# Kernel tuning notes

Hardware: AMD Instinct MI355X
Metric: run time of the kernel (lower is better)

The kernel has to match this reference:

```python
import jax, jax.numpy as jnp
import numpy as np

EPS = 1e-5


def setup_inputs() -> dict:
    key = jax.random.key(0)
    ks = jax.random.split(key, 5)
    N, E, D, L = 10000, 160000, 512, 3
    x = jax.random.normal(ks[0], (N, D), dtype=jnp.float32)
    src = jax.random.randint(ks[1], (E,), 0, N, dtype=jnp.int64)
    dst = jax.random.randint(ks[2], (E,), 0, N, dtype=jnp.int64)
    gamma = jnp.ones((L, D), dtype=jnp.float32)
    beta = jnp.zeros((L, D), dtype=jnp.float32)
    # glorot-ish scale so ReLU stack stays well-conditioned
    W = jax.random.normal(ks[3], (L, D, D), dtype=jnp.float32) * (1.0 / np.sqrt(D))
    b = jnp.zeros((L, D), dtype=jnp.float32)
    return {"x": x, "src": src, "dst": dst, "gamma": gamma, "beta": beta, "W": W, "b": b}


def reference(x, src, dst, gamma, beta, W, b):
    N = x.shape[0]
    ones = jnp.ones(src.shape[0], dtype=x.dtype)
    # DGL GraphConv norm='both': src side uses out-degree, dst side uses in-degree
    out_deg = jnp.clip(jax.ops.segment_sum(ones, src, num_segments=N), 1.0)
    in_deg = jnp.clip(jax.ops.segment_sum(ones, dst, num_segments=N), 1.0)
    src_norm = (out_deg ** -0.5)[:, None]  # [N,1]
    dst_norm = (in_deg ** -0.5)[:, None]   # [N,1]
    n_layers = gamma.shape[0]
    for i in range(n_layers):
        # BatchNorm1d (training mode: batch mean, biased variance)
        mu = jnp.mean(x, axis=0)
        var = jnp.var(x, axis=0)
        x = (x - mu) * jax.lax.rsqrt(var + EPS) * gamma[i] + beta[i]
        h = x * src_norm
        agg = jax.ops.segment_sum(h[src], dst, num_segments=N) * dst_norm
        x = jax.nn.relu(agg @ W[i] + b[i])
    return x
```

## Files before the change

### kernel.cpp

```cpp
#include <hip/hip_runtime.h>
#include <hip/hip_bf16.h>

constexpr int N = 10000;
constexpr int D = 512;
constexpr int E = 160000;
constexpr int L = 3;
constexpr float EPS = 1e-5f;

typedef _Float16 half8 __attribute__((ext_vector_type(8)));
typedef _Float16 half2v __attribute__((ext_vector_type(2)));
typedef float floatx4 __attribute__((ext_vector_type(4)));

__device__ __forceinline__ void glds16(const _Float16* g, _Float16* l) {
    __builtin_amdgcn_global_load_lds(
        (const __attribute__((address_space(1))) uint32_t*)(g),
        (__attribute__((address_space(3))) uint32_t*)(l),
        16, 0, 0);
}

constexpr int DEG_BLOCKS  = (E + 255) / 256;
constexpr int CONV_BLOCKS = 1000;
constexpr int TW_BLOCKS   = L * 256;
constexpr int MEGA_BLOCKS = DEG_BLOCKS + CONV_BLOCKS + TW_BLOCKS;

__global__ __launch_bounds__(256) void mega_setup(
    const int* __restrict__ src, const int* __restrict__ dst,
    const float* __restrict__ x, const float* __restrict__ W,
    int* __restrict__ out_deg, int* __restrict__ in_deg,
    _Float16* __restrict__ x16, float* __restrict__ stats0,
    _Float16* __restrict__ Wt) {
    __shared__ float tb[32][33];
    int bid = blockIdx.x;
    int tid = threadIdx.x;
    if (bid < DEG_BLOCKS) {
        int e = bid * 256 + tid;
        if (e < E) {
            atomicAdd(&out_deg[src[e]], 1);
            atomicAdd(&in_deg[dst[e]], 1);
        }
    } else if (bid < DEG_BLOCKS + CONV_BLOCKS) {
        int b = bid - DEG_BLOCKS;
        int r0 = b * 10;
        int r1 = r0 + 10; if (r1 > N) r1 = N;
        int c2 = tid * 2;
        float s0 = 0.f, s1 = 0.f, q0 = 0.f, q1 = 0.f;
        for (int r = r0; r < r1; ++r) {
            float2 v = *(const float2*)(x + (size_t)r * D + c2);
            s0 += v.x; q0 += v.x * v.x;
            s1 += v.y; q1 += v.y * v.y;
            half2v h; h[0] = (_Float16)v.x; h[1] = (_Float16)v.y;
            *(half2v*)(x16 + (size_t)r * D + c2) = h;
        }
        atomicAdd(&stats0[c2], s0);
        atomicAdd(&stats0[c2 + 1], s1);
        atomicAdd(&stats0[D + c2], q0);
        atomicAdd(&stats0[D + c2 + 1], q1);
    } else {
        int b = bid - DEG_BLOCKS - CONV_BLOCKS;
        int l = b >> 8;
        int t = b & 255;
        int k0 = (t >> 4) * 32, n0 = (t & 15) * 32;
        int tx = tid & 31, ty = tid >> 5;
        const float* Wl = W + (size_t)l * D * D;
        _Float16* Wtl = Wt + (size_t)l * D * D;
        for (int i = 0; i < 32; i += 8)
            tb[ty + i][tx] = Wl[(size_t)(k0 + ty + i) * D + n0 + tx];
        __syncthreads();
        for (int i = 0; i < 32; i += 8)
            Wtl[(size_t)(n0 + ty + i) * D + k0 + tx] = (_Float16)tb[tx][ty + i];
    }
}

__global__ void scan_indeg(const int* __restrict__ in_deg,
                           const int* __restrict__ out_deg,
                           int* __restrict__ off, int* __restrict__ cursor,
                           float* __restrict__ src_norm, float* __restrict__ dst_norm) {
    __shared__ int lsum[1024];
    int t = threadIdx.x;
    const int chunk = (N + 1023) / 1024;
    int start = t * chunk;
    int end = start + chunk; if (end > N) end = N;
    int s = 0;
    for (int i = start; i < end; ++i) s += in_deg[i];
    lsum[t] = s;
    __syncthreads();
    for (int d = 1; d < 1024; d <<= 1) {
        int v = (t >= d) ? lsum[t - d] : 0;
        __syncthreads();
        lsum[t] += v;
        __syncthreads();
    }
    int excl = (t == 0) ? 0 : lsum[t - 1];
    for (int i = start; i < end; ++i) {
        off[i] = excl;
        cursor[i] = excl;
        excl += in_deg[i];
        int od = out_deg[i]; if (od < 1) od = 1;
        int id = in_deg[i];  if (id < 1) id = 1;
        src_norm[i] = rsqrtf((float)od);
        dst_norm[i] = rsqrtf((float)id);
    }
    if (t == 1023) off[N] = lsum[1023];
}

__global__ void csr_fill(const int* __restrict__ src, const int* __restrict__ dst,
                         int* __restrict__ cursor, int* __restrict__ csr_src) {
    int e = blockIdx.x * blockDim.x + threadIdx.x;
    if (e >= E) return;
    int d = dst[e];
    int pos = atomicAdd(&cursor[d], 1);
    csr_src[pos] = src[e];
}

__global__ __launch_bounds__(256) void aggregate_bn(
    const _Float16* __restrict__ x, const int* __restrict__ off,
    const int* __restrict__ csr_src, const float* __restrict__ src_norm,
    const float* __restrict__ dst_norm, const float* __restrict__ stats,
    const float* __restrict__ gamma, const float* __restrict__ beta,
    _Float16* __restrict__ agg) {
    int wid = (blockIdx.x * 256 + threadIdx.x) >> 6;
    if (wid >= N) return;
    int lane = threadIdx.x & 63;
    int c0 = lane * 8;

    float scale[8], shift[8];
    const float invN = 1.0f / (float)N;
    for (int i = 0; i < 8; ++i) {
        int c = c0 + i;
        float mu = stats[c] * invN;
        float var = stats[D + c] * invN - mu * mu;
        float sc = gamma[c] * rsqrtf(var + EPS);
        scale[i] = sc;
        shift[i] = beta[c] - mu * sc;
    }

    int e0 = off[wid], e1 = off[wid + 1];
    float a[8] = {}, a2[8] = {};
    float t = 0.f;
    int e = e0;
    for (; e + 4 <= e1; e += 4) {
        int s0 = csr_src[e];
        int s1 = csr_src[e + 1];
        int s2 = csr_src[e + 2];
        int s3 = csr_src[e + 3];
        float n0 = src_norm[s0];
        float n1 = src_norm[s1];
        float n2 = src_norm[s2];
        float n3 = src_norm[s3];
        half8 v0 = *(const half8*)(x + (size_t)s0 * D + c0);
        half8 v1 = *(const half8*)(x + (size_t)s1 * D + c0);
        half8 v2 = *(const half8*)(x + (size_t)s2 * D + c0);
        half8 v3 = *(const half8*)(x + (size_t)s3 * D + c0);
        t += (n0 + n1) + (n2 + n3);
        for (int k = 0; k < 8; ++k) {
            a[k]  += (float)v0[k] * n0;
            a2[k] += (float)v1[k] * n1;
            a[k]  += (float)v2[k] * n2;
            a2[k] += (float)v3[k] * n3;
        }
    }
    for (; e < e1; ++e) {
        int s0 = csr_src[e];
        float n0 = src_norm[s0];
        half8 v0 = *(const half8*)(x + (size_t)s0 * D + c0);
        t += n0;
        for (int k = 0; k < 8; ++k) a[k] += (float)v0[k] * n0;
    }
    float dn = dst_norm[wid];
    half8 o;
    for (int i = 0; i < 8; ++i)
        o[i] = (_Float16)(dn * (scale[i] * (a[i] + a2[i]) + shift[i] * t));
    *(half8*)(agg + (size_t)wid * D + c0) = o;
}

template <typename OutT, bool STATS>
__global__ __launch_bounds__(128) void mm_f16_relu(
    const _Float16* __restrict__ A, const _Float16* __restrict__ Bt,
    const float* __restrict__ bias, OutT* __restrict__ C, int M,
    float* __restrict__ stats) {
    __shared__ __align__(16) _Float16 As[2][64 * 64];
    __shared__ __align__(16) _Float16 Bs[2][128 * 64];
    const int tid  = threadIdx.x;
    const int wave = tid >> 6;
    const int lane = tid & 63;
    const int quad = lane >> 4;
    const int l16  = lane & 15;
    const int row0 = blockIdx.x * 64;
    const int col0 = blockIdx.y * 128;
    const int wn   = wave * 64;

    const int srl = lane >> 3;
    const int sq  = lane & 7;
    const int sqs = (sq ^ srl) * 8;

    const _Float16* gA[4];
    const _Float16* gB[8];
#pragma unroll
    for (int j = 0; j < 4; ++j) {
        int ar = row0 + wave * 32 + j * 8 + srl;
        if (ar >= M) ar = M - 1;
        gA[j] = A + (size_t)ar * D + sqs;
    }
#pragma unroll
    for (int j = 0; j < 8; ++j) {
        int br = col0 + wave * 64 + j * 8 + srl;
        gB[j] = Bt + (size_t)br * D + sqs;
    }

    const int l7 = l16 & 7;
    const int swz0 = (quad ^ l7) * 8;
    const int swz1 = ((4 + quad) ^ l7) * 8;

    floatx4 acc[4][4] = {};

    auto stage = [&](int buf, int k0) {
        _Float16* as = As[buf] + (wave * 32) * 64;
        _Float16* bs = Bs[buf] + (wave * 64) * 64;
#pragma unroll
        for (int j = 0; j < 4; ++j)
            glds16(gA[j] + k0, as + j * 8 * 64);
#pragma unroll
        for (int j = 0; j < 8; ++j)
            glds16(gB[j] + k0, bs + j * 8 * 64);
    };

    stage(0, 0);
    __syncthreads();

    int cur = 0;
    for (int kt = 0; kt < 8; ++kt) {
        if (kt < 7) stage(cur ^ 1, (kt + 1) * 64);
        const _Float16* asb = As[cur];
        const _Float16* bsb = Bs[cur];
        half8 af0[4], af1[4], bf0[4], bf1[4];
#pragma unroll
        for (int i = 0; i < 4; ++i) {
            int r = i * 16 + l16;
            af0[i] = *(const half8*)(asb + r * 64 + swz0);
            af1[i] = *(const half8*)(asb + r * 64 + swz1);
        }
#pragma unroll
        for (int j = 0; j < 4; ++j) {
            int r = wn + j * 16 + l16;
            bf0[j] = *(const half8*)(bsb + r * 64 + swz0);
            bf1[j] = *(const half8*)(bsb + r * 64 + swz1);
        }
#pragma unroll
        for (int i = 0; i < 4; ++i)
#pragma unroll
            for (int j = 0; j < 4; ++j)
                acc[i][j] = __builtin_amdgcn_mfma_f32_16x16x32_f16(
                    af0[i], bf0[j], acc[i][j], 0, 0, 0);
#pragma unroll
        for (int i = 0; i < 4; ++i)
#pragma unroll
            for (int j = 0; j < 4; ++j)
                acc[i][j] = __builtin_amdgcn_mfma_f32_16x16x32_f16(
                    af1[i], bf1[j], acc[i][j], 0, 0, 0);
        __syncthreads();
        cur ^= 1;
    }

    float s[4] = {}, q[4] = {};
#pragma unroll
    for (int i = 0; i < 4; ++i) {
#pragma unroll
        for (int r = 0; r < 4; ++r) {
            int row = row0 + i * 16 + quad * 4 + r;
            bool valid = row < M;
#pragma unroll
            for (int j = 0; j < 4; ++j) {
                int col = col0 + wn + j * 16 + l16;
                float v = acc[i][j][r] + bias[col];
                v = v > 0.f ? v : 0.f;
                if (valid) {
                    C[(size_t)row * D + col] = (OutT)v;
                    if (STATS) { s[j] += v; q[j] += v * v; }
                }
            }
        }
    }
    if (STATS) {
#pragma unroll
        for (int j = 0; j < 4; ++j) {
            float sv = s[j], qv = q[j];
            sv += __shfl_xor(sv, 16); sv += __shfl_xor(sv, 32);
            qv += __shfl_xor(qv, 16); qv += __shfl_xor(qv, 32);
            if (quad == 0) {
                int col = col0 + wn + j * 16 + l16;
                atomicAdd(&stats[col], sv);
                atomicAdd(&stats[D + col], qv);
            }
        }
    }
}

extern "C" void kernel_launch(void* const* d_in, const int* in_sizes, int n_in,
                              void* d_out, int out_size, void* d_ws, size_t ws_size,
                              hipStream_t stream) {
    const float* x_in  = (const float*)d_in[0];
    const int*   src   = (const int*)d_in[1];
    const int*   dst   = (const int*)d_in[2];
    const float* gamma = (const float*)d_in[3];
    const float* beta  = (const float*)d_in[4];
    const float* W     = (const float*)d_in[5];
    const float* b     = (const float*)d_in[6];
    float* out = (float*)d_out;

    char* p = (char*)d_ws;
    _Float16* x16 = (_Float16*)p;  p += (size_t)N * D * 2;
    _Float16* agg = (_Float16*)p;  p += (size_t)N * D * 2;
    _Float16* Wt  = (_Float16*)p;  p += (size_t)L * D * D * 2;
    float* src_norm = (float*)p;   p += (size_t)N * 4;
    float* dst_norm = (float*)p;   p += (size_t)N * 4;
    int* out_deg   = (int*)p;      p += (size_t)N * 4;
    int* in_deg    = (int*)p;      p += (size_t)N * 4;
    float* stats0  = (float*)p;    p += 2 * D * 4;
    float* stats1  = (float*)p;    p += 2 * D * 4;
    float* stats2  = (float*)p;    p += 2 * D * 4;
    int* csr_off   = (int*)p;      p += (size_t)(N + 1) * 4;
    int* cursor    = (int*)p;      p += (size_t)N * 4;
    int* csr_src   = (int*)p;      p += (size_t)E * 4;

    float* stats_in[3] = {stats0, stats1, stats2};

    hipMemsetAsync(out_deg, 0, (2 * (size_t)N + 6 * D) * sizeof(int), stream);
    mega_setup<<<MEGA_BLOCKS, 256, 0, stream>>>(src, dst, x_in, W,
                                                out_deg, in_deg, x16, stats0, Wt);
    scan_indeg<<<1, 1024, 0, stream>>>(in_deg, out_deg, csr_off, cursor,
                                       src_norm, dst_norm);
    csr_fill<<<DEG_BLOCKS, 256, 0, stream>>>(src, dst, cursor, csr_src);

    dim3 mm_grid((N + 63) / 64, D / 128);
    const int agg_blocks = (N + 3) / 4;

    for (int l = 0; l < L; ++l) {
        const float* gl  = gamma + (size_t)l * D;
        const float* bl  = beta + (size_t)l * D;
        const _Float16* Wl = Wt + (size_t)l * D * D;
        const float* bil = b + (size_t)l * D;

        aggregate_bn<<<agg_blocks, 256, 0, stream>>>(
            x16, csr_off, csr_src, src_norm, dst_norm, stats_in[l], gl, bl, agg);
        if (l == L - 1) {
            mm_f16_relu<float, false><<<mm_grid, 128, 0, stream>>>(
                agg, Wl, bil, out, N, nullptr);
        } else {
            mm_f16_relu<_Float16, true><<<mm_grid, 128, 0, stream>>>(
                agg, Wl, bil, x16, N, stats_in[l + 1]);
        }
    }
}
```

Before: 317.6 us.

## Enlarge GEMM tile to 128x128 with 4 waves and reshuffle setup kernels

The GEMM tile grows from 64x128 with 2 waves to 128x128 with 4 waves arranged 2x2, so each block reuses both A and B tiles more and needs fewer blocks. The setup kernel processes 40 rows per block in the convert/stats branch and orders that branch first. The norm computation moves out of the single-block scan into extra blocks of csr_fill to shorten the serial scan. Some unroll pragmas in the epilogue are removed, which may raise register or indexing overhead, and the larger tile leaves fewer blocks to fill the GPU.

```diff
diff --git a/kernel.cpp b/kernel.cpp
--- a/kernel.cpp
+++ b/kernel.cpp
@@ -18,10 +18,10 @@
         16, 0, 0);
 }
 
+constexpr int CONV_BLOCKS = 250;
 constexpr int DEG_BLOCKS  = (E + 255) / 256;
-constexpr int CONV_BLOCKS = 1000;
 constexpr int TW_BLOCKS   = L * 256;
-constexpr int MEGA_BLOCKS = DEG_BLOCKS + CONV_BLOCKS + TW_BLOCKS;
+constexpr int MEGA_BLOCKS = CONV_BLOCKS + DEG_BLOCKS + TW_BLOCKS;
 
 __global__ __launch_bounds__(256) void mega_setup(
     const int* __restrict__ src, const int* __restrict__ dst,
@@ -32,16 +32,9 @@
     __shared__ float tb[32][33];
     int bid = blockIdx.x;
     int tid = threadIdx.x;
-    if (bid < DEG_BLOCKS) {
-        int e = bid * 256 + tid;
-        if (e < E) {
-            atomicAdd(&out_deg[src[e]], 1);
-            atomicAdd(&in_deg[dst[e]], 1);
-        }
-    } else if (bid < DEG_BLOCKS + CONV_BLOCKS) {
-        int b = bid - DEG_BLOCKS;
-        int r0 = b * 10;
-        int r1 = r0 + 10; if (r1 > N) r1 = N;
+    if (bid < CONV_BLOCKS) {
+        int r0 = bid * 40;
+        int r1 = r0 + 40; if (r1 > N) r1 = N;
         int c2 = tid * 2;
         float s0 = 0.f, s1 = 0.f, q0 = 0.f, q1 = 0.f;
         for (int r = r0; r < r1; ++r) {
@@ -55,8 +48,14 @@
         atomicAdd(&stats0[c2 + 1], s1);
         atomicAdd(&stats0[D + c2], q0);
         atomicAdd(&stats0[D + c2 + 1], q1);
+    } else if (bid < CONV_BLOCKS + DEG_BLOCKS) {
+        int e = (bid - CONV_BLOCKS) * 256 + tid;
+        if (e < E) {
+            atomicAdd(&out_deg[src[e]], 1);
+            atomicAdd(&in_deg[dst[e]], 1);
+        }
     } else {
-        int b = bid - DEG_BLOCKS - CONV_BLOCKS;
+        int b = bid - CONV_BLOCKS - DEG_BLOCKS;
         int l = b >> 8;
         int t = b & 255;
         int k0 = (t >> 4) * 32, n0 = (t & 15) * 32;
@@ -72,9 +71,7 @@
 }
 
 __global__ void scan_indeg(const int* __restrict__ in_deg,
-                           const int* __restrict__ out_deg,
-                           int* __restrict__ off, int* __restrict__ cursor,
-                           float* __restrict__ src_norm, float* __restrict__ dst_norm) {
+                           int* __restrict__ off, int* __restrict__ cursor) {
     __shared__ int lsum[1024];
     int t = threadIdx.x;
     const int chunk = (N + 1023) / 1024;
@@ -95,21 +92,30 @@
         off[i] = excl;
         cursor[i] = excl;
         excl += in_deg[i];
+    }
+    if (t == 1023) off[N] = lsum[1023];
+}
+
+constexpr int NORM_BLOCKS = (N + 255) / 256;
+__global__ void csr_fill(const int* __restrict__ src, const int* __restrict__ dst,
+                         int* __restrict__ cursor, int* __restrict__ csr_src,
+                         const int* __restrict__ in_deg, const int* __restrict__ out_deg,
+                         float* __restrict__ src_norm, float* __restrict__ dst_norm) {
+    int bid = blockIdx.x;
+    if (bid < DEG_BLOCKS) {
+        int e = bid * 256 + threadIdx.x;
+        if (e >= E) return;
+        int d = dst[e];
+        int pos = atomicAdd(&cursor[d], 1);
+        csr_src[pos] = src[e];
+    } else {
+        int i = (bid - DEG_BLOCKS) * 256 + threadIdx.x;
+        if (i >= N) return;
         int od = out_deg[i]; if (od < 1) od = 1;
         int id = in_deg[i];  if (id < 1) id = 1;
         src_norm[i] = rsqrtf((float)od);
         dst_norm[i] = rsqrtf((float)id);
     }
-    if (t == 1023) off[N] = lsum[1023];
-}
-
-__global__ void csr_fill(const int* __restrict__ src, const int* __restrict__ dst,
-                         int* __restrict__ cursor, int* __restrict__ csr_src) {
-    int e = blockIdx.x * blockDim.x + threadIdx.x;
-    if (e >= E) return;
-    int d = dst[e];
-    int pos = atomicAdd(&cursor[d], 1);
-    csr_src[pos] = src[e];
 }
 
 __global__ __launch_bounds__(256) void aggregate_bn(
@@ -174,36 +180,34 @@
 }
 
 template <typename OutT, bool STATS>
-__global__ __launch_bounds__(128) void mm_f16_relu(
+__global__ __launch_bounds__(256) void mm_f16_relu(
     const _Float16* __restrict__ A, const _Float16* __restrict__ Bt,
     const float* __restrict__ bias, OutT* __restrict__ C, int M,
     float* __restrict__ stats) {
-    __shared__ __align__(16) _Float16 As[2][64 * 64];
+    __shared__ __align__(16) _Float16 As[2][128 * 64];
     __shared__ __align__(16) _Float16 Bs[2][128 * 64];
     const int tid  = threadIdx.x;
     const int wave = tid >> 6;
     const int lane = tid & 63;
     const int quad = lane >> 4;
     const int l16  = lane & 15;
-    const int row0 = blockIdx.x * 64;
+    const int row0 = blockIdx.x * 128;
     const int col0 = blockIdx.y * 128;
-    const int wn   = wave * 64;
+    const int wm = (wave & 1) * 64;
+    const int wn = (wave >> 1) * 64;
 
     const int srl = lane >> 3;
     const int sq  = lane & 7;
     const int sqs = (sq ^ srl) * 8;
 
     const _Float16* gA[4];
-    const _Float16* gB[8];
+    const _Float16* gB[4];
 #pragma unroll
     for (int j = 0; j < 4; ++j) {
         int ar = row0 + wave * 32 + j * 8 + srl;
         if (ar >= M) ar = M - 1;
         gA[j] = A + (size_t)ar * D + sqs;
-    }
-#pragma unroll
-    for (int j = 0; j < 8; ++j) {
-        int br = col0 + wave * 64 + j * 8 + srl;
+        int br = col0 + wave * 32 + j * 8 + srl;
         gB[j] = Bt + (size_t)br * D + sqs;
     }
 
@@ -215,13 +219,12 @@
 
     auto stage = [&](int buf, int k0) {
         _Float16* as = As[buf] + (wave * 32) * 64;
-        _Float16* bs = Bs[buf] + (wave * 64) * 64;
-#pragma unroll
-        for (int j = 0; j < 4; ++j)
+        _Float16* bs = Bs[buf] + (wave * 32) * 64;
+#pragma unroll
+        for (int j = 0; j < 4; ++j) {
             glds16(gA[j] + k0, as + j * 8 * 64);
-#pragma unroll
-        for (int j = 0; j < 8; ++j)
             glds16(gB[j] + k0, bs + j * 8 * 64);
+        }
     };
 
     stage(0, 0);
@@ -235,7 +238,7 @@
         half8 af0[4], af1[4], bf0[4], bf1[4];
 #pragma unroll
         for (int i = 0; i < 4; ++i) {
-            int r = i * 16 + l16;
+            int r = wm + i * 16 + l16;
             af0[i] = *(const half8*)(asb + r * 64 + swz0);
             af1[i] = *(const half8*)(asb + r * 64 + swz1);
         }
@@ -262,13 +265,10 @@
     }
 
     float s[4] = {}, q[4] = {};
-#pragma unroll
     for (int i = 0; i < 4; ++i) {
-#pragma unroll
         for (int r = 0; r < 4; ++r) {
-            int row = row0 + i * 16 + quad * 4 + r;
+            int row = row0 + wm + i * 16 + quad * 4 + r;
             bool valid = row < M;
-#pragma unroll
             for (int j = 0; j < 4; ++j) {
                 int col = col0 + wn + j * 16 + l16;
                 float v = acc[i][j][r] + bias[col];
@@ -281,7 +281,6 @@
         }
     }
     if (STATS) {
-#pragma unroll
         for (int j = 0; j < 4; ++j) {
             float sv = s[j], qv = q[j];
             sv += __shfl_xor(sv, 16); sv += __shfl_xor(sv, 32);
@@ -327,11 +326,11 @@
     hipMemsetAsync(out_deg, 0, (2 * (size_t)N + 6 * D) * sizeof(int), stream);
     mega_setup<<<MEGA_BLOCKS, 256, 0, stream>>>(src, dst, x_in, W,
                                                 out_deg, in_deg, x16, stats0, Wt);
-    scan_indeg<<<1, 1024, 0, stream>>>(in_deg, out_deg, csr_off, cursor,
-                                       src_norm, dst_norm);
-    csr_fill<<<DEG_BLOCKS, 256, 0, stream>>>(src, dst, cursor, csr_src);
-
-    dim3 mm_grid((N + 63) / 64, D / 128);
+    scan_indeg<<<1, 1024, 0, stream>>>(in_deg, csr_off, cursor);
+    csr_fill<<<DEG_BLOCKS + NORM_BLOCKS, 256, 0, stream>>>(
+        src, dst, cursor, csr_src, in_deg, out_deg, src_norm, dst_norm);
+
+    dim3 mm_grid((N + 127) / 128, D / 128);
     const int agg_blocks = (N + 3) / 4;
 
     for (int l = 0; l < L; ++l) {
@@ -343,10 +342,10 @@
         aggregate_bn<<<agg_blocks, 256, 0, stream>>>(
             x16, csr_off, csr_src, src_norm, dst_norm, stats_in[l], gl, bl, agg);
         if (l == L - 1) {
-            mm_f16_relu<float, false><<<mm_grid, 128, 0, stream>>>(
+            mm_f16_relu<float, false><<<mm_grid, 256, 0, stream>>>(
                 agg, Wl, bil, out, N, nullptr);
         } else {
-            mm_f16_relu<_Float16, true><<<mm_grid, 128, 0, stream>>>(
+            mm_f16_relu<_Float16, true><<<mm_grid, 256, 0, stream>>>(
                 agg, Wl, bil, x16, N, stats_in[l + 1]);
         }
     }
```

New measurement: 283.9 us. -10.6%, faster.
